# Performance work log

Measured on AMD Instinct MI355X. Metric: run time of the kernel, lower is better.

## Reference

```python
import jax, jax.numpy as jnp
import numpy as np

N_NODES = 20000
N_EDGES = 160000
IN_DIM = 512
HID = 256
N_CLASSES = 2
NUM_GRAPHS = 16


def setup_inputs() -> dict:
    key = jax.random.key(0)
    ks = jax.random.split(key, 12)
    x = jax.random.normal(ks[0], (N_NODES, IN_DIM), dtype=jnp.float32)
    edge_index = jax.random.randint(ks[1], (2, N_EDGES), 0, N_NODES, dtype=jnp.int64)
    batch = jnp.sort(jax.random.randint(ks[2], (N_NODES,), 0, NUM_GRAPHS, dtype=jnp.int64))
    def glorot(k, shape):
        lim = float(np.sqrt(6.0 / (shape[0] + shape[1])))
        return jax.random.uniform(k, shape, jnp.float32, -lim, lim)
    return {
        "x": x,
        "edge_index": edge_index,
        "batch": batch,
        "W1n": glorot(ks[3], (IN_DIM, HID)),
        "W1s": glorot(ks[4], (IN_DIM, HID)),
        "b1": jnp.zeros((HID,), jnp.float32),
        "W2n": glorot(ks[5], (HID, HID)),
        "W2s": glorot(ks[6], (HID, HID)),
        "b2": jnp.zeros((HID,), jnp.float32),
        "fc1w": glorot(ks[7], (HID, HID // 2)),
        "fc1b": jnp.zeros((HID // 2,), jnp.float32),
        "fc2w": glorot(ks[8], (HID // 2, N_CLASSES)),
        "fc2b": jnp.zeros((N_CLASSES,), jnp.float32),
    }


def _sage_conv(x, W_nbr, W_self, b, src, dst, n_nodes):
    # mean-aggregate neighbor features (messages flow src -> dst, PyG convention)
    deg = jax.ops.segment_sum(jnp.ones(src.shape, x.dtype), dst, num_segments=n_nodes)
    deg = jnp.maximum(deg, 1.0)
    aggr = jax.ops.segment_sum(x[src], dst, num_segments=n_nodes) / deg[:, None]
    # SAGEConv: lin_l(aggr) + lin_r(x) + bias (equivalent to concat-linear)
    return aggr @ W_nbr + x @ W_self + b


def reference(x, edge_index, batch, W1n, W1s, b1, W2n, W2s, b2, fc1w, fc1b, fc2w, fc2b):
    src, dst = edge_index[0], edge_index[1]
    n = x.shape[0]
    h = jax.nn.relu(_sage_conv(x, W1n, W1s, b1, src, dst, n))
    h = jax.nn.relu(_sage_conv(h, W2n, W2s, b2, src, dst, n))
    # global_mean_pool over graph ids
    cnt = jax.ops.segment_sum(jnp.ones((n,), h.dtype), batch, num_segments=NUM_GRAPHS)
    pooled = jax.ops.segment_sum(h, batch, num_segments=NUM_GRAPHS) / jnp.maximum(cnt, 1.0)[:, None]
    out = jax.nn.relu(pooled @ fc1w + fc1b) @ fc2w + fc2b
    return out
```

## Files before the change

### kernel.cpp

```cpp
#include <hip/hip_runtime.h>
#include <hip/hip_bf16.h>


#define HID 256
#define NCOL 512

typedef __bf16 bf16x8 __attribute__((ext_vector_type(8)));
typedef float floatx4 __attribute__((ext_vector_type(4)));
typedef unsigned int u32;
typedef const u32 __attribute__((address_space(1)))* gp_t;
typedef u32 __attribute__((address_space(3)))* lp_t;

__device__ __forceinline__ ushort f2bf(float f) {
    unsigned u = __float_as_uint(f);
    u += 0x7fffu + ((u >> 16) & 1u);
    return (ushort)(u >> 16);
}
__device__ __forceinline__ float bf2f(ushort b) {
    return __uint_as_float(((unsigned)b) << 16);
}

__device__ __forceinline__ void packT_work(const float* __restrict__ Wn,
                                           const float* __restrict__ Ws,
                                           ushort* __restrict__ WT, int K, int gid) {
    if (gid >= NCOL * K) return;
    int n = gid / K, k = gid - n * K;
    float v = (n < HID) ? Wn[k * HID + n] : Ws[k * HID + (n - HID)];
    WT[gid] = f2bf(v);
}

__global__ void prep_kernel(const float* __restrict__ x, ushort* __restrict__ xb, int n4,
                            const float* __restrict__ W1n, const float* __restrict__ W1s,
                            ushort* __restrict__ w1t, int K1,
                            const float* __restrict__ W2n, const float* __restrict__ W2s,
                            ushort* __restrict__ w2t, int K2,
                            const int* __restrict__ dst, int* __restrict__ degi, int n_edges,
                            int nb_cvt, int nb_w1, int nb_w2) {
    int bx = blockIdx.x, t = threadIdx.x;
    if (bx < nb_cvt) {
        int i = bx * 256 + t;
        if (i < n4) {
            float4 v = ((const float4*)x)[i];
            ushort4 o;
            o.x = f2bf(v.x); o.y = f2bf(v.y); o.z = f2bf(v.z); o.w = f2bf(v.w);
            ((ushort4*)xb)[i] = o;
        }
    } else if (bx < nb_cvt + nb_w1) {
        packT_work(W1n, W1s, w1t, K1, (bx - nb_cvt) * 256 + t);
    } else if (bx < nb_cvt + nb_w1 + nb_w2) {
        packT_work(W2n, W2s, w2t, K2, (bx - nb_cvt - nb_w1) * 256 + t);
    } else {
        int e = (bx - nb_cvt - nb_w1 - nb_w2) * 256 + t;
        if (e < n_edges) atomicAdd(&degi[dst[e]], 1);
    }
}

__global__ __launch_bounds__(256) void psum_kernel(const int* __restrict__ degi,
                                                   int* __restrict__ partials, int n) {
    int t = threadIdx.x;
    int i = blockIdx.x * 256 + t;
    int v = (i < n) ? degi[i] : 0;
#pragma unroll
    for (int d = 1; d < 64; d <<= 1) v += __shfl_xor(v, d, 64);
    __shared__ int wsum[4];
    if ((t & 63) == 0) wsum[t >> 6] = v;
    __syncthreads();
    if (t == 0) partials[blockIdx.x] = wsum[0] + wsum[1] + wsum[2] + wsum[3];
}

__global__ __launch_bounds__(256) void scan2_kernel(const int* __restrict__ degi,
                                                    const int* __restrict__ partials,
                                                    int* __restrict__ off,
                                                    int* __restrict__ cursor, int n, int nb) {
    int t = threadIdx.x, lane = t & 63, w = t >> 6;
    int c = blockIdx.x;
    int pre = 0, tot = 0;
    for (int base = 0; base < nb; base += 64) {
        int idx = base + lane;
        int pv = (idx < nb) ? partials[idx] : 0;
        pre += (idx < c) ? pv : 0;
        tot += pv;
    }
#pragma unroll
    for (int d = 1; d < 64; d <<= 1) {
        pre += __shfl_xor(pre, d, 64);
        tot += __shfl_xor(tot, d, 64);
    }
    if (c == 0 && t == 0) off[n] = tot;
    int i = c * 256 + t;
    int v = (i < n) ? degi[i] : 0;
    int s = v;
#pragma unroll
    for (int d = 1; d < 64; d <<= 1) {
        int u = __shfl_up(s, d, 64);
        if (lane >= d) s += u;
    }
    __shared__ int wsum[4];
    if (lane == 63) wsum[w] = s;
    __syncthreads();
    int woff = 0;
    for (int k = 0; k < w; ++k) woff += wsum[k];
    int excl = pre + woff + s - v;
    if (i < n) { off[i] = excl; cursor[i] = excl; }
}

__global__ void fill_kernel(const int* __restrict__ src, const int* __restrict__ dst,
                            int* __restrict__ cursor, int* __restrict__ eidx, int n_edges) {
    int e = blockIdx.x * 256 + threadIdx.x;
    if (e < n_edges) {
        int p = atomicAdd(&cursor[dst[e]], 1);
        eidx[p] = src[e];
    }
}

__global__ __launch_bounds__(256) void gemm_mfma(const ushort* __restrict__ A,
                                                 const ushort* __restrict__ BT,
                                                 ushort* __restrict__ Y, int K, int nG) {
    int b = blockIdx.x;
    int xcd = b & 7, rest = b >> 3;
    int m = rest & 3, Ggrp = rest >> 2;
    int G = xcd + 8 * Ggrp;
    if (G >= nG) return;
    int m0 = G * 64, n0 = m * 128;

    __shared__ ushort As[2][64 * 64];
    __shared__ ushort Bs[2][128 * 64];
    int tid = threadIdx.x;
    int w = tid >> 6, lane = tid & 63;
    int quad = lane >> 4, r16 = lane & 15;
    int wm = (w >> 1) * 32, wn = (w & 1) * 64;

    int arow[2], agu[2], brow[4], bgu[4];
#pragma unroll
    for (int rr = 0; rr < 2; ++rr) {
        int idx = rr * 256 + tid;
        arow[rr] = idx >> 3;
        agu[rr] = (idx & 7) ^ (arow[rr] & 7);
    }
#pragma unroll
    for (int rr = 0; rr < 4; ++rr) {
        int idx = rr * 256 + tid;
        brow[rr] = idx >> 3;
        bgu[rr] = (idx & 7) ^ (brow[rr] & 7);
    }

    auto stage = [&](int buf, int k0) {
#pragma unroll
        for (int rr = 0; rr < 2; ++rr) {
            const ushort* ga = A + (size_t)(m0 + arow[rr]) * K + k0 + agu[rr] * 8;
            ushort* la = As[buf] + (size_t)(rr * 256 + w * 64) * 8;
            __builtin_amdgcn_global_load_lds((gp_t)(const void*)ga, (lp_t)(void*)la, 16, 0, 0);
        }
#pragma unroll
        for (int rr = 0; rr < 4; ++rr) {
            const ushort* gb = BT + (size_t)(n0 + brow[rr]) * K + k0 + bgu[rr] * 8;
            ushort* lb = Bs[buf] + (size_t)(rr * 256 + w * 64) * 8;
            __builtin_amdgcn_global_load_lds((gp_t)(const void*)gb, (lp_t)(void*)lb, 16, 0, 0);
        }
    };

    floatx4 acc[2][4];
#pragma unroll
    for (int i = 0; i < 2; ++i)
#pragma unroll
        for (int j = 0; j < 4; ++j) acc[i][j] = (floatx4){0.f, 0.f, 0.f, 0.f};

    const int nk = K >> 6;
    stage(0, 0);
    for (int t = 0; t < nk; ++t) {
        int cb = t & 1;
        __syncthreads();
        if (t + 1 < nk) stage(cb ^ 1, (t + 1) << 6);
        const ushort* Ab = As[cb];
        const ushort* Bb = Bs[cb];
#pragma unroll
        for (int s = 0; s < 2; ++s) {
            bf16x8 a[2], b2[4];
#pragma unroll
            for (int i = 0; i < 2; ++i) {
                int row = wm + i * 16 + r16;
                int au = (s * 4 + quad) ^ (row & 7);
                a[i] = *(const bf16x8*)(Ab + row * 64 + au * 8);
            }
#pragma unroll
            for (int j = 0; j < 4; ++j) {
                int row = wn + j * 16 + r16;
                int bu = (s * 4 + quad) ^ (row & 7);
                b2[j] = *(const bf16x8*)(Bb + row * 64 + bu * 8);
            }
#pragma unroll
            for (int i = 0; i < 2; ++i)
#pragma unroll
                for (int j = 0; j < 4; ++j)
                    acc[i][j] = __builtin_amdgcn_mfma_f32_16x16x32_bf16(a[i], b2[j], acc[i][j], 0, 0, 0);
        }
    }
#pragma unroll
    for (int i = 0; i < 2; ++i)
#pragma unroll
        for (int j = 0; j < 4; ++j) {
            int col = n0 + wn + j * 16 + r16;
#pragma unroll
            for (int rg = 0; rg < 4; ++rg) {
                int row = m0 + wm + i * 16 + quad * 4 + rg;
                Y[(size_t)row * NCOL + col] = f2bf(acc[i][j][rg]);
            }
        }
}

#define ACC4(A, Yv) { A.x += bf2f(Yv.x); A.y += bf2f(Yv.y); A.z += bf2f(Yv.z); A.w += bf2f(Yv.w); }
__global__ __launch_bounds__(256) void gather_kernel(const ushort* __restrict__ Y,
                                                     const int* __restrict__ off,
                                                     const int* __restrict__ eidx,
                                                     const float* __restrict__ bias,
                                                     ushort* __restrict__ h, int n_nodes) {
    int tid = threadIdx.x;
    int v = blockIdx.x * 4 + (tid >> 6);
    if (v >= n_nodes) return;
    int lane = tid & 63;
    int q4 = lane << 2;
    int e0 = off[v], e1 = off[v + 1];
    ushort4 sv = *(const ushort4*)(Y + (size_t)v * NCOL + HID + q4);
    float4 b = *(const float4*)(bias + q4);
    float4 a0 = make_float4(0.f, 0.f, 0.f, 0.f), a1 = a0, a2 = a0, a3 = a0;
    for (int base = e0; base < e1; base += 64) {
        int ecnt = min(64, e1 - base);
        int ev = (lane < ecnt) ? eidx[base + lane] : 0;
        int j = 0;
        for (; j + 8 <= ecnt; j += 8) {
            int s0 = __shfl(ev, j + 0), s1 = __shfl(ev, j + 1);
            int s2 = __shfl(ev, j + 2), s3 = __shfl(ev, j + 3);
            int s4 = __shfl(ev, j + 4), s5 = __shfl(ev, j + 5);
            int s6 = __shfl(ev, j + 6), s7 = __shfl(ev, j + 7);
            ushort4 y0 = *(const ushort4*)(Y + (size_t)s0 * NCOL + q4);
            ushort4 y1 = *(const ushort4*)(Y + (size_t)s1 * NCOL + q4);
            ushort4 y2 = *(const ushort4*)(Y + (size_t)s2 * NCOL + q4);
            ushort4 y3 = *(const ushort4*)(Y + (size_t)s3 * NCOL + q4);
            ushort4 y4 = *(const ushort4*)(Y + (size_t)s4 * NCOL + q4);
            ushort4 y5 = *(const ushort4*)(Y + (size_t)s5 * NCOL + q4);
            ushort4 y6 = *(const ushort4*)(Y + (size_t)s6 * NCOL + q4);
            ushort4 y7 = *(const ushort4*)(Y + (size_t)s7 * NCOL + q4);
            ACC4(a0, y0); ACC4(a1, y1); ACC4(a2, y2); ACC4(a3, y3);
            ACC4(a0, y4); ACC4(a1, y5); ACC4(a2, y6); ACC4(a3, y7);
        }
        for (; j < ecnt; ++j) {
            int s = __shfl(ev, j);
            ushort4 y = *(const ushort4*)(Y + (size_t)s * NCOL + q4);
            ACC4(a0, y);
        }
    }
    float invd = 1.0f / fmaxf((float)(e1 - e0), 1.0f);
    ushort4 r;
    r.x = f2bf(fmaxf((a0.x + a1.x + a2.x + a3.x) * invd + bf2f(sv.x) + b.x, 0.f));
    r.y = f2bf(fmaxf((a0.y + a1.y + a2.y + a3.y) * invd + bf2f(sv.y) + b.y, 0.f));
    r.z = f2bf(fmaxf((a0.z + a1.z + a2.z + a3.z) * invd + bf2f(sv.z) + b.z, 0.f));
    r.w = f2bf(fmaxf((a0.w + a1.w + a2.w + a3.w) * invd + bf2f(sv.w) + b.w, 0.f));
    *(ushort4*)(h + (size_t)v * HID + q4) = r;
}

__global__ void pool_kernel(const ushort* __restrict__ h, const int* __restrict__ batch,
                            float* __restrict__ pooled, float* __restrict__ cnt, int n_nodes) {
    int f = threadIdx.x;
    int v0 = blockIdx.x * 64;
    int vend = min(v0 + 64, n_nodes);
    if (v0 >= n_nodes) return;
    int cur = batch[v0];
    float acc = 0.f, ac = 0.f;
    for (int v = v0; v < vend; ++v) {
        int g = batch[v];
        if (g != cur) {
            atomicAdd(&pooled[cur * HID + f], acc);
            if (f == 0) atomicAdd(&cnt[cur], ac);
            acc = 0.f; ac = 0.f; cur = g;
        }
        acc += bf2f(h[(size_t)v * HID + f]);
        ac += 1.0f;
    }
    atomicAdd(&pooled[cur * HID + f], acc);
    if (f == 0) atomicAdd(&cnt[cur], ac);
}

__global__ void head_kernel(const float* __restrict__ pooled, const float* __restrict__ cnt,
                            const float* __restrict__ fc1w, const float* __restrict__ fc1b,
                            const float* __restrict__ fc2w, const float* __restrict__ fc2b,
                            float* __restrict__ out) {
    int g = blockIdx.x, j = threadIdx.x;
    __shared__ float p[256];
    __shared__ float hid[128];
    float inv = 1.0f / fmaxf(cnt[g], 1.0f);
    p[j] = pooled[g * HID + j] * inv;
    p[j + 128] = pooled[g * HID + 128 + j] * inv;
    __syncthreads();
    float a = fc1b[j];
    for (int f = 0; f < 256; ++f) a += p[f] * fc1w[f * 128 + j];
    hid[j] = fmaxf(a, 0.f);
    __syncthreads();
    if (j < 2) {
        float o = fc2b[j];
        for (int t = 0; t < 128; ++t) o += hid[t] * fc2w[t * 2 + j];
        out[g * 2 + j] = o;
    }
}

extern "C" void kernel_launch(void* const* d_in, const int* in_sizes, int n_in,
                              void* d_out, int out_size, void* d_ws, size_t ws_size,
                              hipStream_t stream) {
    const float* x    = (const float*)d_in[0];
    const int*   ei   = (const int*)d_in[1];
    const int*   batch= (const int*)d_in[2];
    const float* W1n  = (const float*)d_in[3];
    const float* W1s  = (const float*)d_in[4];
    const float* b1   = (const float*)d_in[5];
    const float* W2n  = (const float*)d_in[6];
    const float* W2s  = (const float*)d_in[7];
    const float* b2   = (const float*)d_in[8];
    const float* fc1w = (const float*)d_in[9];
    const float* fc1b = (const float*)d_in[10];
    const float* fc2w = (const float*)d_in[11];
    const float* fc2b = (const float*)d_in[12];
    float* out = (float*)d_out;

    const int n_nodes = in_sizes[2];
    const int n_edges = in_sizes[1] / 2;
    const int in_dim  = in_sizes[0] / n_nodes;
    const int Mpad    = (n_nodes + 63) & ~63;
    const int nb      = (n_nodes + 255) / 256;
    const int nG      = Mpad / 64;
    const int* src = ei;
    const int* dst = ei + n_edges;

    char* wsb = (char*)d_ws;
    size_t cur = 0;
    auto alloc = [&](size_t nbytes) { size_t o = cur; cur = (cur + nbytes + 255) & ~(size_t)255; return o; };
    size_t o_degi = alloc((size_t)n_nodes * 4);
    size_t o_off  = alloc((size_t)(n_nodes + 1) * 4);
    size_t o_cur  = alloc((size_t)n_nodes * 4);
    size_t o_part = alloc((size_t)nb * 4);
    size_t o_eidx = alloc((size_t)n_edges * 4);
    size_t o_w1   = alloc((size_t)NCOL * in_dim * 2);
    size_t o_w2   = alloc((size_t)NCOL * HID * 2);
    size_t o_xb   = alloc((size_t)Mpad * in_dim * 2);
    size_t o_hb   = alloc((size_t)Mpad * HID * 2);
    size_t o_y    = alloc((size_t)Mpad * NCOL * 2);
    size_t o_pool = alloc((size_t)16 * HID * 4 + 16 * 4);
    (void)ws_size;

    int*    degi    = (int*)(wsb + o_degi);
    int*    off     = (int*)(wsb + o_off);
    int*    cursor  = (int*)(wsb + o_cur);
    int*    partials= (int*)(wsb + o_part);
    int*    eidx    = (int*)(wsb + o_eidx);
    ushort* w1t     = (ushort*)(wsb + o_w1);
    ushort* w2t     = (ushort*)(wsb + o_w2);
    ushort* xb      = (ushort*)(wsb + o_xb);
    ushort* hb      = (ushort*)(wsb + o_hb);
    ushort* Y       = (ushort*)(wsb + o_y);
    float*  pooled  = (float*)(wsb + o_pool);
    float*  cnt     = pooled + 16 * HID;

    hipMemsetAsync(degi, 0, (size_t)n_nodes * 4, stream);
    hipMemsetAsync(pooled, 0, (size_t)(16 * HID + 16) * 4, stream);

    int n4 = n_nodes * in_dim / 4;
    int nb_cvt = (n4 + 255) / 256;
    int nb_w1  = (NCOL * in_dim + 255) / 256;
    int nb_w2  = (NCOL * HID + 255) / 256;
    int nb_deg = (n_edges + 255) / 256;
    prep_kernel<<<nb_cvt + nb_w1 + nb_w2 + nb_deg, 256, 0, stream>>>(
        x, xb, n4, W1n, W1s, w1t, in_dim, W2n, W2s, w2t, HID,
        dst, degi, n_edges, nb_cvt, nb_w1, nb_w2);

    psum_kernel<<<nb, 256, 0, stream>>>(degi, partials, n_nodes);
    scan2_kernel<<<nb, 256, 0, stream>>>(degi, partials, off, cursor, n_nodes, nb);
    fill_kernel<<<(n_edges + 255) / 256, 256, 0, stream>>>(src, dst, cursor, eidx, n_edges);

    int gemm_blocks = 8 * 4 * ((nG + 7) / 8);
    int gather_blocks = (n_nodes + 3) / 4;

    gemm_mfma<<<gemm_blocks, 256, 0, stream>>>(xb, w1t, Y, in_dim, nG);
    gather_kernel<<<gather_blocks, 256, 0, stream>>>(Y, off, eidx, b1, hb, n_nodes);

    gemm_mfma<<<gemm_blocks, 256, 0, stream>>>(hb, w2t, Y, HID, nG);
    gather_kernel<<<gather_blocks, 256, 0, stream>>>(Y, off, eidx, b2, hb, n_nodes);

    pool_kernel<<<(n_nodes + 63) / 64, 256, 0, stream>>>(hb, batch, pooled, cnt, n_nodes);
    head_kernel<<<16, 128, 0, stream>>>(pooled, cnt, fc1w, fc1b, fc2w, fc2b, out);
}
```

Before: 224.1 us.

## Fuse pooling into gather, single-block scan, 128-row GEMM tiles, merged memset

```diff
diff --git a/kernel.cpp b/kernel.cpp
--- a/kernel.cpp
+++ b/kernel.cpp
@@ -55,53 +55,34 @@
     }
 }
 
-__global__ __launch_bounds__(256) void psum_kernel(const int* __restrict__ degi,
-                                                   int* __restrict__ partials, int n) {
+__global__ __launch_bounds__(1024) void scan_kernel(const int* __restrict__ degi,
+                                                    int* __restrict__ off,
+                                                    int* __restrict__ cursor, int n) {
     int t = threadIdx.x;
-    int i = blockIdx.x * 256 + t;
-    int v = (i < n) ? degi[i] : 0;
-#pragma unroll
-    for (int d = 1; d < 64; d <<= 1) v += __shfl_xor(v, d, 64);
-    __shared__ int wsum[4];
-    if ((t & 63) == 0) wsum[t >> 6] = v;
-    __syncthreads();
-    if (t == 0) partials[blockIdx.x] = wsum[0] + wsum[1] + wsum[2] + wsum[3];
-}
-
-__global__ __launch_bounds__(256) void scan2_kernel(const int* __restrict__ degi,
-                                                    const int* __restrict__ partials,
-                                                    int* __restrict__ off,
-                                                    int* __restrict__ cursor, int n, int nb) {
-    int t = threadIdx.x, lane = t & 63, w = t >> 6;
-    int c = blockIdx.x;
-    int pre = 0, tot = 0;
-    for (int base = 0; base < nb; base += 64) {
-        int idx = base + lane;
-        int pv = (idx < nb) ? partials[idx] : 0;
-        pre += (idx < c) ? pv : 0;
-        tot += pv;
-    }
+    const int CH = (n + 1023) >> 10;
+    int lo = t * CH, hi = min(lo + CH, n);
+    if (lo > n) lo = n;
+    if (hi < lo) hi = lo;
+    int s = 0;
+    for (int i = lo; i < hi; ++i) s += degi[i];
+    int lane = t & 63, w = t >> 6;
+    int v = s;
 #pragma unroll
     for (int d = 1; d < 64; d <<= 1) {
-        pre += __shfl_xor(pre, d, 64);
-        tot += __shfl_xor(tot, d, 64);
-    }
-    if (c == 0 && t == 0) off[n] = tot;
-    int i = c * 256 + t;
-    int v = (i < n) ? degi[i] : 0;
-    int s = v;
-#pragma unroll
-    for (int d = 1; d < 64; d <<= 1) {
-        int u = __shfl_up(s, d, 64);
-        if (lane >= d) s += u;
-    }
-    __shared__ int wsum[4];
-    if (lane == 63) wsum[w] = s;
+        int u = __shfl_up(v, d, 64);
+        if (lane >= d) v += u;
+    }
+    __shared__ int wsum[16];
+    if (lane == 63) wsum[w] = v;
     __syncthreads();
     int woff = 0;
     for (int k = 0; k < w; ++k) woff += wsum[k];
-    int excl = pre + woff + s - v;
-    if (i < n) { off[i] = excl; cursor[i] = excl; }
+    int excl = woff + v - s;
+    if (t == 1023) off[n] = excl + s;
+    int run = excl;
+    for (int i = lo; i < hi; ++i) {
+        off[i] = run; cursor[i] = run; run += degi[i];
+    }
 }
 
 __global__ void fill_kernel(const int* __restrict__ src, const int* __restrict__ dst,
@@ -121,47 +102,41 @@
     int m = rest & 3, Ggrp = rest >> 2;
     int G = xcd + 8 * Ggrp;
     if (G >= nG) return;
-    int m0 = G * 64, n0 = m * 128;
-
-    __shared__ ushort As[2][64 * 64];
+    int m0 = G * 128, n0 = m * 128;
+
+    __shared__ ushort As[2][128 * 64];
     __shared__ ushort Bs[2][128 * 64];
     int tid = threadIdx.x;
     int w = tid >> 6, lane = tid & 63;
     int quad = lane >> 4, r16 = lane & 15;
-    int wm = (w >> 1) * 32, wn = (w & 1) * 64;
-
-    int arow[2], agu[2], brow[4], bgu[4];
-#pragma unroll
-    for (int rr = 0; rr < 2; ++rr) {
+    int wm = (w >> 1) * 64, wn = (w & 1) * 64;
+
+    int arow[4], agu[4];
+#pragma unroll
+    for (int rr = 0; rr < 4; ++rr) {
         int idx = rr * 256 + tid;
         arow[rr] = idx >> 3;
         agu[rr] = (idx & 7) ^ (arow[rr] & 7);
     }
-#pragma unroll
-    for (int rr = 0; rr < 4; ++rr) {
-        int idx = rr * 256 + tid;
-        brow[rr] = idx >> 3;
-        bgu[rr] = (idx & 7) ^ (brow[rr] & 7);
-    }
 
     auto stage = [&](int buf, int k0) {
 #pragma unroll
-        for (int rr = 0; rr < 2; ++rr) {
+        for (int rr = 0; rr < 4; ++rr) {
             const ushort* ga = A + (size_t)(m0 + arow[rr]) * K + k0 + agu[rr] * 8;
             ushort* la = As[buf] + (size_t)(rr * 256 + w * 64) * 8;
             __builtin_amdgcn_global_load_lds((gp_t)(const void*)ga, (lp_t)(void*)la, 16, 0, 0);
         }
 #pragma unroll
         for (int rr = 0; rr < 4; ++rr) {
-            const ushort* gb = BT + (size_t)(n0 + brow[rr]) * K + k0 + bgu[rr] * 8;
+            const ushort* gb = BT + (size_t)(n0 + arow[rr]) * K + k0 + agu[rr] * 8;
             ushort* lb = Bs[buf] + (size_t)(rr * 256 + w * 64) * 8;
             __builtin_amdgcn_global_load_lds((gp_t)(const void*)gb, (lp_t)(void*)lb, 16, 0, 0);
         }
     };
 
-    floatx4 acc[2][4];
-#pragma unroll
-    for (int i = 0; i < 2; ++i)
+    floatx4 acc[4][4];
+#pragma unroll
+    for (int i = 0; i < 4; ++i)
 #pragma unroll
         for (int j = 0; j < 4; ++j) acc[i][j] = (floatx4){0.f, 0.f, 0.f, 0.f};
 
@@ -175,9 +150,9 @@
         const ushort* Bb = Bs[cb];
 #pragma unroll
         for (int s = 0; s < 2; ++s) {
-            bf16x8 a[2], b2[4];
-#pragma unroll
-            for (int i = 0; i < 2; ++i) {
+            bf16x8 a[4], bfr[4];
+#pragma unroll
+            for (int i = 0; i < 4; ++i) {
                 int row = wm + i * 16 + r16;
                 int au = (s * 4 + quad) ^ (row & 7);
                 a[i] = *(const bf16x8*)(Ab + row * 64 + au * 8);
@@ -186,17 +161,17 @@
             for (int j = 0; j < 4; ++j) {
                 int row = wn + j * 16 + r16;
                 int bu = (s * 4 + quad) ^ (row & 7);
-                b2[j] = *(const bf16x8*)(Bb + row * 64 + bu * 8);
+                bfr[j] = *(const bf16x8*)(Bb + row * 64 + bu * 8);
             }
 #pragma unroll
-            for (int i = 0; i < 2; ++i)
+            for (int i = 0; i < 4; ++i)
 #pragma unroll
                 for (int j = 0; j < 4; ++j)
-                    acc[i][j] = __builtin_amdgcn_mfma_f32_16x16x32_bf16(a[i], b2[j], acc[i][j], 0, 0, 0);
-        }
-    }
-#pragma unroll
-    for (int i = 0; i < 2; ++i)
+                    acc[i][j] = __builtin_amdgcn_mfma_f32_16x16x32_bf16(a[i], bfr[j], acc[i][j], 0, 0, 0);
+        }
+    }
+#pragma unroll
+    for (int i = 0; i < 4; ++i)
 #pragma unroll
         for (int j = 0; j < 4; ++j) {
             int col = n0 + wn + j * 16 + r16;
@@ -209,11 +184,16 @@
 }
 
 #define ACC4(A, Yv) { A.x += bf2f(Yv.x); A.y += bf2f(Yv.y); A.z += bf2f(Yv.z); A.w += bf2f(Yv.w); }
+template<int POOL>
 __global__ __launch_bounds__(256) void gather_kernel(const ushort* __restrict__ Y,
                                                      const int* __restrict__ off,
                                                      const int* __restrict__ eidx,
                                                      const float* __restrict__ bias,
-                                                     ushort* __restrict__ h, int n_nodes) {
+                                                     ushort* __restrict__ h,
+                                                     const int* __restrict__ batch,
+                                                     float* __restrict__ pooled,
+                                                     float* __restrict__ cnt,
+                                                     int n_nodes) {
     int tid = threadIdx.x;
     int v = blockIdx.x * 4 + (tid >> 6);
     if (v >= n_nodes) return;
@@ -250,34 +230,23 @@
         }
     }
     float invd = 1.0f / fmaxf((float)(e1 - e0), 1.0f);
-    ushort4 r;
-    r.x = f2bf(fmaxf((a0.x + a1.x + a2.x + a3.x) * invd + bf2f(sv.x) + b.x, 0.f));
-    r.y = f2bf(fmaxf((a0.y + a1.y + a2.y + a3.y) * invd + bf2f(sv.y) + b.y, 0.f));
-    r.z = f2bf(fmaxf((a0.z + a1.z + a2.z + a3.z) * invd + bf2f(sv.z) + b.z, 0.f));
-    r.w = f2bf(fmaxf((a0.w + a1.w + a2.w + a3.w) * invd + bf2f(sv.w) + b.w, 0.f));
-    *(ushort4*)(h + (size_t)v * HID + q4) = r;
-}
-
-__global__ void pool_kernel(const ushort* __restrict__ h, const int* __restrict__ batch,
-                            float* __restrict__ pooled, float* __restrict__ cnt, int n_nodes) {
-    int f = threadIdx.x;
-    int v0 = blockIdx.x * 64;
-    int vend = min(v0 + 64, n_nodes);
-    if (v0 >= n_nodes) return;
-    int cur = batch[v0];
-    float acc = 0.f, ac = 0.f;
-    for (int v = v0; v < vend; ++v) {
+    float r0 = fmaxf((a0.x + a1.x + a2.x + a3.x) * invd + bf2f(sv.x) + b.x, 0.f);
+    float r1 = fmaxf((a0.y + a1.y + a2.y + a3.y) * invd + bf2f(sv.y) + b.y, 0.f);
+    float r2 = fmaxf((a0.z + a1.z + a2.z + a3.z) * invd + bf2f(sv.z) + b.z, 0.f);
+    float r3 = fmaxf((a0.w + a1.w + a2.w + a3.w) * invd + bf2f(sv.w) + b.w, 0.f);
+    if (POOL) {
         int g = batch[v];
-        if (g != cur) {
-            atomicAdd(&pooled[cur * HID + f], acc);
-            if (f == 0) atomicAdd(&cnt[cur], ac);
-            acc = 0.f; ac = 0.f; cur = g;
-        }
-        acc += bf2f(h[(size_t)v * HID + f]);
-        ac += 1.0f;
-    }
-    atomicAdd(&pooled[cur * HID + f], acc);
-    if (f == 0) atomicAdd(&cnt[cur], ac);
+        float* pg = pooled + (size_t)g * HID + q4;
+        atomicAdd(pg + 0, r0);
+        atomicAdd(pg + 1, r1);
+        atomicAdd(pg + 2, r2);
+        atomicAdd(pg + 3, r3);
+        if (lane == 0) atomicAdd(&cnt[g], 1.0f);
+    } else {
+        ushort4 r;
+        r.x = f2bf(r0); r.y = f2bf(r1); r.z = f2bf(r2); r.w = f2bf(r3);
+        *(ushort4*)(h + (size_t)v * HID + q4) = r;
+    }
 }
 
 __global__ void head_kernel(const float* __restrict__ pooled, const float* __restrict__ cnt,
@@ -323,9 +292,8 @@
     const int n_nodes = in_sizes[2];
     const int n_edges = in_sizes[1] / 2;
     const int in_dim  = in_sizes[0] / n_nodes;
-    const int Mpad    = (n_nodes + 63) & ~63;
-    const int nb      = (n_nodes + 255) / 256;
-    const int nG      = Mpad / 64;
+    const int Mpad    = (n_nodes + 127) & ~127;
+    const int nG      = Mpad / 128;
     const int* src = ei;
     const int* dst = ei + n_edges;
 
@@ -333,33 +301,31 @@
     size_t cur = 0;
     auto alloc = [&](size_t nbytes) { size_t o = cur; cur = (cur + nbytes + 255) & ~(size_t)255; return o; };
     size_t o_degi = alloc((size_t)n_nodes * 4);
+    size_t o_pool = alloc((size_t)16 * HID * 4 + 16 * 4);
+    size_t zero_end = cur;
     size_t o_off  = alloc((size_t)(n_nodes + 1) * 4);
     size_t o_cur  = alloc((size_t)n_nodes * 4);
-    size_t o_part = alloc((size_t)nb * 4);
     size_t o_eidx = alloc((size_t)n_edges * 4);
     size_t o_w1   = alloc((size_t)NCOL * in_dim * 2);
     size_t o_w2   = alloc((size_t)NCOL * HID * 2);
     size_t o_xb   = alloc((size_t)Mpad * in_dim * 2);
     size_t o_hb   = alloc((size_t)Mpad * HID * 2);
     size_t o_y    = alloc((size_t)Mpad * NCOL * 2);
-    size_t o_pool = alloc((size_t)16 * HID * 4 + 16 * 4);
     (void)ws_size;
 
     int*    degi    = (int*)(wsb + o_degi);
+    float*  pooled  = (float*)(wsb + o_pool);
+    float*  cnt     = pooled + 16 * HID;
     int*    off     = (int*)(wsb + o_off);
     int*    cursor  = (int*)(wsb + o_cur);
-    int*    partials= (int*)(wsb + o_part);
     int*    eidx    = (int*)(wsb + o_eidx);
     ushort* w1t     = (ushort*)(wsb + o_w1);
     ushort* w2t     = (ushort*)(wsb + o_w2);
     ushort* xb      = (ushort*)(wsb + o_xb);
     ushort* hb      = (ushort*)(wsb + o_hb);
     ushort* Y       = (ushort*)(wsb + o_y);
-    float*  pooled  = (float*)(wsb + o_pool);
-    float*  cnt     = pooled + 16 * HID;
-
-    hipMemsetAsync(degi, 0, (size_t)n_nodes * 4, stream);
-    hipMemsetAsync(pooled, 0, (size_t)(16 * HID + 16) * 4, stream);
+
+    hipMemsetAsync(wsb + o_degi, 0, zero_end - o_degi, stream);
 
     int n4 = n_nodes * in_dim / 4;
     int nb_cvt = (n4 + 255) / 256;
@@ -370,19 +336,19 @@
         x, xb, n4, W1n, W1s, w1t, in_dim, W2n, W2s, w2t, HID,
         dst, degi, n_edges, nb_cvt, nb_w1, nb_w2);
 
-    psum_kernel<<<nb, 256, 0, stream>>>(degi, partials, n_nodes);
-    scan2_kernel<<<nb, 256, 0, stream>>>(degi, partials, off, cursor, n_nodes, nb);
+    scan_kernel<<<1, 1024, 0, stream>>>(degi, off, cursor, n_nodes);
     fill_kernel<<<(n_edges + 255) / 256, 256, 0, stream>>>(src, dst, cursor, eidx, n_edges);
 
     int gemm_blocks = 8 * 4 * ((nG + 7) / 8);
     int gather_blocks = (n_nodes + 3) / 4;
 
     gemm_mfma<<<gemm_blocks, 256, 0, stream>>>(xb, w1t, Y, in_dim, nG);
-    gather_kernel<<<gather_blocks, 256, 0, stream>>>(Y, off, eidx, b1, hb, n_nodes);
+    gather_kernel<0><<<gather_blocks, 256, 0, stream>>>(Y, off, eidx, b1, hb,
+                                                        nullptr, nullptr, nullptr, n_nodes);
 
     gemm_mfma<<<gemm_blocks, 256, 0, stream>>>(hb, w2t, Y, HID, nG);
-    gather_kernel<<<gather_blocks, 256, 0, stream>>>(Y, off, eidx, b2, hb, n_nodes);
-
-    pool_kernel<<<(n_nodes + 63) / 64, 256, 0, stream>>>(hb, batch, pooled, cnt, n_nodes);
+    gather_kernel<1><<<gather_blocks, 256, 0, stream>>>(Y, off, eidx, b2, nullptr,
+                                                        batch, pooled, cnt, n_nodes);
+
     head_kernel<<<16, 128, 0, stream>>>(pooled, cnt, fc1w, fc1b, fc2w, fc2b, out);
 }
```

Measured after the change: 522.4 us. +133.1%, slower.
